# Kernel optimization log

Measured on AMD Instinct MI355X. Metric: run time of the kernel, lower is better.

Reference implementation:

```python
import jax, jax.numpy as jnp
import numpy as np

B, S, D, H = 2, 2048, 1024, 16
HD = D // H  # head dim = 64


def setup_inputs() -> dict:
    key = jax.random.key(0)
    ks = jax.random.split(key, 11)
    s = 0.02
    return {
        "query": jax.random.normal(ks[0], (B, S, D), jnp.float32),
        "key": jax.random.normal(ks[1], (B, S, D), jnp.float32),
        "value": jax.random.normal(ks[2], (B, S, D), jnp.float32),
        "Wq": jax.random.normal(ks[3], (D, D), jnp.float32) * s,
        "bq": jnp.zeros((D,), jnp.float32),
        "Wk": jax.random.normal(ks[4], (D, D), jnp.float32) * s,
        "bk": jnp.zeros((D,), jnp.float32),
        "Wv": jax.random.normal(ks[5], (D, D), jnp.float32) * s,
        "bv": jnp.zeros((D,), jnp.float32),
        "Wo": jax.random.normal(ks[6], (D, D), jnp.float32) * s,
        "bo": jnp.zeros((D,), jnp.float32),
    }


def reference(query, key, value, Wq, bq, Wk, bk, Wv, bv, Wo, bo):
    # Linear projections (torch Linear: x @ W^T + b; here W stored as [in, out])
    q = query @ Wq + bq  # [B,S,D]
    k = key @ Wk + bk
    v = value @ Wv + bv
    # split heads -> [B,H,S,HD]
    q = q.reshape(B, S, H, HD).transpose(0, 2, 1, 3)
    k = k.reshape(B, S, H, HD).transpose(0, 2, 1, 3)
    v = v.reshape(B, S, H, HD).transpose(0, 2, 1, 3)
    scores = jnp.einsum("bhqd,bhkd->bhqk", q, k) / jnp.sqrt(jnp.float32(HD))
    probs = jax.nn.softmax(scores, axis=-1)
    # dropout is identity at inference
    ctx = jnp.einsum("bhqk,bhkd->bhqd", probs, v)
    ctx = ctx.transpose(0, 2, 1, 3).reshape(B, S, D)
    return ctx @ Wo + bo
```

## Files before the change

kernel.cpp:

```cpp
#include <hip/hip_runtime.h>
#include <hip/hip_bf16.h>

#define BB 2
#define SS 2048
#define DD 1024
#define HH 16
#define HD 64
#define MM (BB*SS)

typedef __attribute__((ext_vector_type(8))) short bf16x8;
typedef __attribute__((ext_vector_type(4))) float f32x4;

static __device__ inline unsigned short f2bf(float x) {
    unsigned int u = __float_as_uint(x);
    unsigned int r = (u + 0x7fffu + ((u >> 16) & 1u)) >> 16;
    return (unsigned short)r;
}

static __device__ inline unsigned pack2bf(float lo, float hi) {
    union { __hip_bfloat162 h; unsigned u; } c;
    c.h = __float22bfloat162_rn(make_float2(lo, hi));
    return c.u;
}

static __device__ inline f32x4 mfma16(bf16x8 a, bf16x8 b, f32x4 c) {
    return __builtin_amdgcn_mfma_f32_16x16x32_bf16(a, b, c, 0, 0, 0);
}

static __device__ inline float fast_exp2(float x) {
    return __builtin_amdgcn_exp2f(x);
}

typedef __attribute__((address_space(3))) unsigned int lds_u32;
typedef const __attribute__((address_space(1))) unsigned int glb_u32;
static __device__ inline void async_ld16(const void* g, void* l) {
    __builtin_amdgcn_global_load_lds((glb_u32*)g, (lds_u32*)l, 16, 0, 0);
}

struct PrepArgs {
    const float* csrc[3];
    unsigned short* cdst[3];
    const float* wsrc[4];
    unsigned short* wdst[4];
};
__global__ __launch_bounds__(256) void prep_inputs(PrepArgs args) {
    const int z = blockIdx.z;
    const int t = threadIdx.x;
    if (z < 3) {
        const float* in = args.csrc[z];
        unsigned short* out = args.cdst[z];
        int chunk = (blockIdx.y * 32 + blockIdx.x) * 4096;
#pragma unroll
        for (int r = 0; r < 4; r++) {
            int i = chunk + r * 1024 + t * 4;
            float4 v = *(const float4*)(in + i);
            uint2 o;
            o.x = pack2bf(v.x, v.y);
            o.y = pack2bf(v.z, v.w);
            *(uint2*)(out + i) = o;
        }
    } else {
        __shared__ float tile[32][33];
        const float* in = args.wsrc[z - 3];
        unsigned short* out = args.wdst[z - 3];
        int c0 = blockIdx.x * 32, r0 = blockIdx.y * 32;
        int x = t & 31, y0 = t >> 5;
        for (int yy = y0; yy < 32; yy += 8)
            tile[yy][x] = in[(size_t)(r0 + yy) * DD + c0 + x];
        __syncthreads();
        for (int yy = y0; yy < 32; yy += 8)
            out[(size_t)(c0 + yy) * DD + r0 + x] = f2bf(tile[x][yy]);
    }
}

struct QKVArgs {
    const unsigned short* A[3];
    const unsigned short* Bt[3];
    const float* bias[3];
    unsigned short* C[3];
};

#define QSCALE 0.1803368801111204f

#define NBUF 4
#define NT (DD / 32)

__global__ __launch_bounds__(512, 2) void gemm_qkv(QKVArgs args) {
    __shared__ alignas(16) unsigned short AS[NBUF][256 * 32];
    __shared__ alignas(16) unsigned short BS[NBUF][256 * 32];
    const int z = blockIdx.z;
    const float scale = (z == 0) ? QSCALE : 1.0f;
    const unsigned short* __restrict__ A = args.A[z];
    const unsigned short* __restrict__ Bt = args.Bt[z];
    const float* __restrict__ bias = args.bias[z];
    unsigned short* __restrict__ C = args.C[z];
    const int K = DD, N = DD;
    const int t = threadIdx.x;
    const int lane = t & 63, wave = t >> 6;
    const int quad = lane >> 4, l15 = lane & 15;
    const int wm = wave & 1, wn = wave >> 1;
    const int m0 = blockIdx.y * 256, n0 = blockIdx.x * 256;

    const int srow = wave * 16 + (lane >> 2);
    const int sslot = (lane & 3) ^ ((lane >> 3) & 3);
    const unsigned short* gA0 = A + (size_t)(m0 + srow) * K + sslot * 8;
    const unsigned short* gA1 = gA0 + (size_t)128 * K;
    const unsigned short* gB0 = Bt + (size_t)(n0 + srow) * K + sslot * 8;
    const unsigned short* gB1 = gB0 + (size_t)128 * K;
    const int rlo = wave * 512;
    const int rhi = wave * 512 + 4096;

    const int swzq = quad ^ ((l15 >> 1) & 3);

    auto stage = [&](int kt) {
        const int b = kt & (NBUF - 1);
        const size_t ko = (size_t)kt * 32;
        async_ld16(gA0 + ko, &AS[b][rlo]);
        async_ld16(gA1 + ko, &AS[b][rhi]);
        async_ld16(gB0 + ko, &BS[b][rlo]);
        async_ld16(gB1 + ko, &BS[b][rhi]);
    };

    stage(0); stage(1); stage(2);

    f32x4 acc[8][4];
#pragma unroll
    for (int i = 0; i < 8; i++)
#pragma unroll
        for (int j = 0; j < 4; j++) acc[i][j] = (f32x4){0.f, 0.f, 0.f, 0.f};

#pragma unroll 4
    for (int kt = 0; kt < NT; ++kt) {
        if (kt < NT - 2)       asm volatile("s_waitcnt vmcnt(8)" ::: "memory");
        else if (kt == NT - 2) asm volatile("s_waitcnt vmcnt(4)" ::: "memory");
        else                   asm volatile("s_waitcnt vmcnt(0)" ::: "memory");
        __builtin_amdgcn_s_barrier();
        if (kt + 3 < NT) stage(kt + 3);

        const unsigned short* Ab = AS[kt & (NBUF - 1)];
        const unsigned short* Bb = BS[kt & (NBUF - 1)];
        bf16x8 af[8], bfr[4];
#pragma unroll
        for (int i = 0; i < 8; i++)
            af[i] = *(const bf16x8*)&Ab[(wm * 128 + i * 16 + l15) * 32 + swzq * 8];
#pragma unroll
        for (int j = 0; j < 4; j++)
            bfr[j] = *(const bf16x8*)&Bb[(wn * 64 + j * 16 + l15) * 32 + swzq * 8];

        __builtin_amdgcn_s_setprio(1);
#pragma unroll
        for (int i = 0; i < 8; i++)
#pragma unroll
            for (int j = 0; j < 4; j++)
                acc[i][j] = mfma16(af[i], bfr[j], acc[i][j]);
        __builtin_amdgcn_s_setprio(0);
    }

    if (z == 2) {
#pragma unroll
        for (int j = 0; j < 4; j++) {
            int col = n0 + wn * 64 + j * 16 + l15;
            float bv = bias[col];
#pragma unroll
            for (int i = 0; i < 8; i++) {
                int rowb = m0 + wm * 128 + i * 16 + quad * 4;
                int b = rowb >> 11, s = rowb & (SS - 1);
                uint2 w;
                w.x = pack2bf(acc[i][j][0] + bv, acc[i][j][1] + bv);
                w.y = pack2bf(acc[i][j][2] + bv, acc[i][j][3] + bv);
                *(uint2*)(C + (size_t)b * DD * SS + (size_t)col * SS + s) = w;
            }
        }
    } else {
#pragma unroll
        for (int j = 0; j < 4; j++) {
            int col = n0 + wn * 64 + j * 16 + l15;
            float bv = bias[col];
#pragma unroll
            for (int i = 0; i < 8; i++) {
                int rowb = m0 + wm * 128 + i * 16 + quad * 4;
#pragma unroll
                for (int rr = 0; rr < 4; rr++) {
                    float v = (acc[i][j][rr] + bv) * scale;
                    C[(size_t)(rowb + rr) * N + col] = f2bf(v);
                }
            }
        }
    }
}

__global__ __launch_bounds__(256) void gemm_out(const unsigned short* __restrict__ A,
                                                const unsigned short* __restrict__ Bt,
                                                const float* __restrict__ bias,
                                                float* __restrict__ C) {
    __shared__ alignas(16) unsigned short As[128 * 32];
    __shared__ alignas(16) unsigned short Bs[64 * 32];
    const int t = threadIdx.x;
    const int lane = t & 63, wave = t >> 6;
    const int quad = lane >> 4, l15 = lane & 15;
    const int m0 = blockIdx.y * 128, n0 = blockIdx.x * 64;
    const int K = DD, N = DD;

    const unsigned short* gA = A + (size_t)(m0 + wave * 16 + (lane >> 2)) * K + (lane & 3) * 8;
    const unsigned short* gB = Bt + (size_t)(n0 + wave * 16 + (lane >> 2)) * K + (lane & 3) * 8;
    unsigned short* lA0 = &As[(wave * 16) * 32];
    unsigned short* lA1 = &As[(wave * 16 + 64) * 32];
    unsigned short* lB0 = &Bs[(wave * 16) * 32];

    f32x4 acc[2][4];
#pragma unroll
    for (int i = 0; i < 2; i++)
#pragma unroll
        for (int j = 0; j < 4; j++) acc[i][j] = (f32x4){0.f, 0.f, 0.f, 0.f};

    for (int k0 = 0; k0 < K; k0 += 32) {
        __syncthreads();
        async_ld16(gA + k0, lA0);
        async_ld16(gA + (size_t)64 * K + k0, lA1);
        async_ld16(gB + k0, lB0);
        __syncthreads();

        bf16x8 af[2], bfr[4];
#pragma unroll
        for (int i = 0; i < 2; i++)
            af[i] = *(const bf16x8*)&As[(wave * 32 + i * 16 + l15) * 32 + quad * 8];
#pragma unroll
        for (int j = 0; j < 4; j++)
            bfr[j] = *(const bf16x8*)&Bs[(j * 16 + l15) * 32 + quad * 8];
#pragma unroll
        for (int i = 0; i < 2; i++)
#pragma unroll
            for (int j = 0; j < 4; j++)
                acc[i][j] = mfma16(af[i], bfr[j], acc[i][j]);
    }

#pragma unroll
    for (int j = 0; j < 4; j++) {
        int col = n0 + j * 16 + l15;
        float bv = bias[col];
#pragma unroll
        for (int i = 0; i < 2; i++) {
            int rowb = m0 + wave * 32 + i * 16 + quad * 4;
#pragma unroll
            for (int rr = 0; rr < 4; rr++)
                C[(size_t)(rowb + rr) * N + col] = acc[i][j][rr] + bv;
        }
    }
}

#define TK 64
#define NTILE (SS / TK)
#define LDP 72

__global__ __launch_bounds__(256, 2) void flash_attn(const unsigned short* __restrict__ Q,
                                                     const unsigned short* __restrict__ Kg,
                                                     const unsigned short* __restrict__ Vt,
                                                     unsigned short* __restrict__ ctx) {
    __shared__ alignas(16) unsigned short Ks[2][TK * LDP];
    __shared__ alignas(16) unsigned short Vs[2][TK * LDP];
    const int t = threadIdx.x;
    const int lane = t & 63, wave = t >> 6;
    const int quad = lane >> 4, l15 = lane & 15;
    const int qg = blockIdx.x & 15;
    const int bh = blockIdx.x >> 4;
    const int h = bh & 15, b = bh >> 4;
    const int q0 = (qg * 4 + wave) * 32;

    const unsigned short* Qb = Q + (size_t)b * SS * DD + h * HD;
    const unsigned short* Kb = Kg + (size_t)b * SS * DD + h * HD;
    const unsigned short* Vb = Vt + ((size_t)b * DD + h * HD) * SS;

    const int r0 = t >> 3, cs = t & 7;
    const unsigned short* gK = Kb + (size_t)r0 * DD + cs * 8;
    const unsigned short* gV = Vb + (size_t)r0 * SS + cs * 8;
    const int ldsoff0 = r0 * LDP + cs * 8;
    const int ldsoff1 = (r0 + 32) * LDP + cs * 8;

    bf16x8 qa[2][2];
#pragma unroll
    for (int qt = 0; qt < 2; qt++) {
        qa[qt][0] = *(const bf16x8*)(Qb + (size_t)(q0 + qt * 16 + l15) * DD + quad * 8);
        qa[qt][1] = *(const bf16x8*)(Qb + (size_t)(q0 + qt * 16 + l15) * DD + 32 + quad * 8);
    }

    float lrow[2] = {0.f, 0.f};
    f32x4 o[2][4];
#pragma unroll
    for (int qt = 0; qt < 2; qt++)
#pragma unroll
        for (int j = 0; j < 4; j++) o[qt][j] = (f32x4){0.f, 0.f, 0.f, 0.f};

    {
        uint4 kr0 = *(const uint4*)(gK);
        uint4 kr1 = *(const uint4*)(gK + (size_t)32 * DD);
        uint4 vr0 = *(const uint4*)(gV);
        uint4 vr1 = *(const uint4*)(gV + (size_t)32 * SS);
        *(uint4*)&Ks[0][ldsoff0] = kr0;
        *(uint4*)&Ks[0][ldsoff1] = kr1;
        *(uint4*)&Vs[0][ldsoff0] = vr0;
        *(uint4*)&Vs[0][ldsoff1] = vr1;
    }
    __syncthreads();

    for (int tile = 0; tile < NTILE; ++tile) {
        const int buf = tile & 1;
        uint4 kr0, kr1, vr0, vr1;
        if (tile + 1 < NTILE) {
            const unsigned short* gKn = gK + (size_t)(tile + 1) * TK * DD;
            const unsigned short* gVn = gV + (tile + 1) * TK;
            kr0 = *(const uint4*)(gKn);
            kr1 = *(const uint4*)(gKn + (size_t)32 * DD);
            vr0 = *(const uint4*)(gVn);
            vr1 = *(const uint4*)(gVn + (size_t)32 * SS);
        }
        const unsigned short* Ksb = Ks[buf];
        const unsigned short* Vsb = Vs[buf];
#pragma unroll
        for (int half = 0; half < 2; half++) {
            const int kb0 = half * 32;
            bf16x8 k0 = *(const bf16x8*)&Ksb[(kb0 + l15) * LDP + quad * 8];
            bf16x8 k1 = *(const bf16x8*)&Ksb[(kb0 + l15) * LDP + 32 + quad * 8];
            bf16x8 k2 = *(const bf16x8*)&Ksb[(kb0 + 16 + l15) * LDP + quad * 8];
            bf16x8 k3 = *(const bf16x8*)&Ksb[(kb0 + 16 + l15) * LDP + 32 + quad * 8];
            union { ushort4 s[2]; bf16x8 v; } af[4];
#pragma unroll
            for (int j = 0; j < 4; j++) {
                af[j].s[0] = *(const ushort4*)&Vsb[(j * 16 + l15) * LDP + kb0 + quad * 4];
                af[j].s[1] = *(const ushort4*)&Vsb[(j * 16 + l15) * LDP + kb0 + 16 + quad * 4];
            }
#pragma unroll
            for (int qt = 0; qt < 2; qt++) {
                f32x4 sc0 = (f32x4){0.f, 0.f, 0.f, 0.f};
                f32x4 sc1 = (f32x4){0.f, 0.f, 0.f, 0.f};
                sc0 = mfma16(k0, qa[qt][0], sc0);
                sc0 = mfma16(k1, qa[qt][1], sc0);
                sc1 = mfma16(k2, qa[qt][0], sc1);
                sc1 = mfma16(k3, qa[qt][1], sc1);

                float p[8];
#pragma unroll
                for (int rr = 0; rr < 4; rr++) {
                    p[rr]     = fast_exp2(sc0[rr]);
                    p[rr + 4] = fast_exp2(sc1[rr]);
                }
                lrow[qt] += (p[0] + p[1]) + (p[2] + p[3]) + (p[4] + p[5]) + (p[6] + p[7]);

                union { unsigned u[4]; bf16x8 v; } pf;
                pf.u[0] = pack2bf(p[0], p[1]);
                pf.u[1] = pack2bf(p[2], p[3]);
                pf.u[2] = pack2bf(p[4], p[5]);
                pf.u[3] = pack2bf(p[6], p[7]);

#pragma unroll
                for (int j = 0; j < 4; j++)
                    o[qt][j] = mfma16(af[j].v, pf.v, o[qt][j]);
            }
        }
        if (tile + 1 < NTILE) {
            __syncthreads();
            *(uint4*)&Ks[buf ^ 1][ldsoff0] = kr0;
            *(uint4*)&Ks[buf ^ 1][ldsoff1] = kr1;
            *(uint4*)&Vs[buf ^ 1][ldsoff0] = vr0;
            *(uint4*)&Vs[buf ^ 1][ldsoff1] = vr1;
            __syncthreads();
        }
    }

#pragma unroll
    for (int qt = 0; qt < 2; qt++) {
        float l = lrow[qt];
        l += __shfl_xor(l, 16, 64);
        l += __shfl_xor(l, 32, 64);
        float linv = 1.0f / l;
        unsigned short* crow = ctx + ((size_t)b * SS + q0 + qt * 16 + l15) * DD + h * HD;
#pragma unroll
        for (int j = 0; j < 4; j++) {
            uint2 w;
            w.x = pack2bf(o[qt][j][0] * linv, o[qt][j][1] * linv);
            w.y = pack2bf(o[qt][j][2] * linv, o[qt][j][3] * linv);
            *(uint2*)(crow + j * 16 + quad * 4) = w;
        }
    }
}

extern "C" void kernel_launch(void* const* d_in, const int* in_sizes, int n_in,
                              void* d_out, int out_size, void* d_ws, size_t ws_size,
                              hipStream_t stream) {
    const float* query = (const float*)d_in[0];
    const float* key   = (const float*)d_in[1];
    const float* value = (const float*)d_in[2];
    const float* Wq = (const float*)d_in[3];
    const float* bq = (const float*)d_in[4];
    const float* Wk = (const float*)d_in[5];
    const float* bk = (const float*)d_in[6];
    const float* Wv = (const float*)d_in[7];
    const float* bv = (const float*)d_in[8];
    const float* Wo = (const float*)d_in[9];
    const float* bo = (const float*)d_in[10];
    float* out = (float*)d_out;

    char* ws = (char*)d_ws;
    const size_t WSZ = (size_t)DD * DD * 2;
    const size_t XSZ = (size_t)MM * DD * 2;
    unsigned short* Wqt = (unsigned short*)(ws + 0 * WSZ);
    unsigned short* Wkt = (unsigned short*)(ws + 1 * WSZ);
    unsigned short* Wvt = (unsigned short*)(ws + 2 * WSZ);
    unsigned short* Wot = (unsigned short*)(ws + 3 * WSZ);
    unsigned short* Xq  = (unsigned short*)(ws + 4 * WSZ);
    unsigned short* Xk  = (unsigned short*)(ws + 4 * WSZ + 1 * XSZ);
    unsigned short* Xv  = (unsigned short*)(ws + 4 * WSZ + 2 * XSZ);
    unsigned short* Qp  = (unsigned short*)(ws + 4 * WSZ + 3 * XSZ);
    unsigned short* Kp  = (unsigned short*)(ws + 4 * WSZ + 4 * XSZ);
    unsigned short* Vtp = (unsigned short*)(ws + 4 * WSZ + 5 * XSZ);
    unsigned short* ctx = Xk;

    PrepArgs pargs;
    pargs.csrc[0] = query; pargs.csrc[1] = key; pargs.csrc[2] = value;
    pargs.cdst[0] = Xq; pargs.cdst[1] = Xk; pargs.cdst[2] = Xv;
    pargs.wsrc[0] = Wq; pargs.wsrc[1] = Wk; pargs.wsrc[2] = Wv; pargs.wsrc[3] = Wo;
    pargs.wdst[0] = Wqt; pargs.wdst[1] = Wkt; pargs.wdst[2] = Wvt; pargs.wdst[3] = Wot;
    prep_inputs<<<dim3(32, 32, 7), 256, 0, stream>>>(pargs);

    QKVArgs args;
    args.A[0] = Xq; args.A[1] = Xk; args.A[2] = Xv;
    args.Bt[0] = Wqt; args.Bt[1] = Wkt; args.Bt[2] = Wvt;
    args.bias[0] = bq; args.bias[1] = bk; args.bias[2] = bv;
    args.C[0] = Qp; args.C[1] = Kp; args.C[2] = Vtp;
    gemm_qkv<<<dim3(DD / 256, MM / 256, 3), 512, 0, stream>>>(args);

    flash_attn<<<BB * HH * 16, 256, 0, stream>>>(Qp, Kp, Vtp, ctx);

    gemm_out<<<dim3(DD / 64, MM / 128), 256, 0, stream>>>(ctx, Wot, bo, out);
}
```

Baseline: 230.8 us.

## Restructure QKV GEMM into 64-wide K tiles with interleaved load/MFMA phases

Replaces the 4-deep 32-wide K-tile ring buffer in the QKV projection GEMM with a double buffer of 64-wide K tiles. Each iteration is split into four quarter phases that read LDS fragments, issue async global loads for the next B or A halves, and run MFMA sub-blocks separated by barriers. This is an HK/8-wave ping-pong style schedule meant to overlap LDS reads, global prefetch and matrix math and to halve loop overhead. It adds many more barriers per iteration and uses a reworked XOR swizzle. The tighter buffer reuse risks races or stalls if the vmcnt accounting is off.

After: 227.6 us. Within noise of the previous version (-1.4%).

```diff
diff --git a/kernel.cpp b/kernel.cpp
--- a/kernel.cpp
+++ b/kernel.cpp
@@ -82,12 +82,11 @@
 
 #define QSCALE 0.1803368801111204f
 
-#define NBUF 4
-#define NT (DD / 32)
+#define NKT 16
 
 __global__ __launch_bounds__(512, 2) void gemm_qkv(QKVArgs args) {
-    __shared__ alignas(16) unsigned short AS[NBUF][256 * 32];
-    __shared__ alignas(16) unsigned short BS[NBUF][256 * 32];
+    __shared__ alignas(16) unsigned short AS[2][256 * 64];
+    __shared__ alignas(16) unsigned short BS[2][256 * 64];
     const int z = blockIdx.z;
     const float scale = (z == 0) ? QSCALE : 1.0f;
     const unsigned short* __restrict__ A = args.A[z];
@@ -101,27 +100,27 @@
     const int wm = wave & 1, wn = wave >> 1;
     const int m0 = blockIdx.y * 256, n0 = blockIdx.x * 256;
 
-    const int srow = wave * 16 + (lane >> 2);
-    const int sslot = (lane & 3) ^ ((lane >> 3) & 3);
-    const unsigned short* gA0 = A + (size_t)(m0 + srow) * K + sslot * 8;
-    const unsigned short* gA1 = gA0 + (size_t)128 * K;
-    const unsigned short* gB0 = Bt + (size_t)(n0 + srow) * K + sslot * 8;
-    const unsigned short* gB1 = gB0 + (size_t)128 * K;
-    const int rlo = wave * 512;
-    const int rhi = wave * 512 + 4096;
-
-    const int swzq = quad ^ ((l15 >> 1) & 3);
-
-    auto stage = [&](int kt) {
-        const int b = kt & (NBUF - 1);
-        const size_t ko = (size_t)kt * 32;
-        async_ld16(gA0 + ko, &AS[b][rlo]);
-        async_ld16(gA1 + ko, &AS[b][rhi]);
-        async_ld16(gB0 + ko, &BS[b][rlo]);
-        async_ld16(gB1 + ko, &BS[b][rhi]);
+    const int srow = t >> 3;
+    const int cslot = (t & 7) ^ (srow & 7);
+    const unsigned short* gA = A + (size_t)(m0 + srow) * K + cslot * 8;
+    const unsigned short* gB = Bt + (size_t)(n0 + srow) * K + cslot * 8;
+    const int dstoff = srow * 64 + (t & 7) * 8;
+
+    auto stageA = [&](int tl, int h) {
+        unsigned short* d = &AS[tl & 1][h * 128 * 64 + dstoff];
+        const unsigned short* s = gA + (size_t)(h * 128) * K + (size_t)tl * 64;
+        async_ld16(s, d);
+        async_ld16(s + (size_t)64 * K, d + 64 * 64);
     };
-
-    stage(0); stage(1); stage(2);
+    auto stageB = [&](int tl, int h) {
+        unsigned short* d = &BS[tl & 1][h * 128 * 64 + dstoff];
+        const unsigned short* s = gB + (size_t)(h * 128) * K + (size_t)tl * 64;
+        async_ld16(s, d);
+        async_ld16(s + (size_t)64 * K, d + 64 * 64);
+    };
+
+    stageA(0, 0); stageA(0, 1); stageB(0, 0); stageB(0, 1);
+    stageA(1, 0); stageA(1, 1);
 
     f32x4 acc[8][4];
 #pragma unroll
@@ -129,30 +128,93 @@
 #pragma unroll
         for (int j = 0; j < 4; j++) acc[i][j] = (f32x4){0.f, 0.f, 0.f, 0.f};
 
-#pragma unroll 4
-    for (int kt = 0; kt < NT; ++kt) {
-        if (kt < NT - 2)       asm volatile("s_waitcnt vmcnt(8)" ::: "memory");
-        else if (kt == NT - 2) asm volatile("s_waitcnt vmcnt(4)" ::: "memory");
-        else                   asm volatile("s_waitcnt vmcnt(0)" ::: "memory");
-        __builtin_amdgcn_s_barrier();
-        if (kt + 3 < NT) stage(kt + 3);
-
-        const unsigned short* Ab = AS[kt & (NBUF - 1)];
-        const unsigned short* Bb = BS[kt & (NBUF - 1)];
-        bf16x8 af[8], bfr[4];
-#pragma unroll
-        for (int i = 0; i < 8; i++)
-            af[i] = *(const bf16x8*)&Ab[(wm * 128 + i * 16 + l15) * 32 + swzq * 8];
-#pragma unroll
-        for (int j = 0; j < 4; j++)
-            bfr[j] = *(const bf16x8*)&Bb[(wn * 64 + j * 16 + l15) * 32 + swzq * 8];
-
+#pragma unroll 2
+    for (int kt = 0; kt < NKT; ++kt) {
+        if (kt < NKT - 1) asm volatile("s_waitcnt vmcnt(4)" ::: "memory");
+        else              asm volatile("s_waitcnt vmcnt(0)" ::: "memory");
+        __builtin_amdgcn_s_barrier();
+
+        const unsigned short* Ab = AS[kt & 1];
+        const unsigned short* Bb = BS[kt & 1];
+        bf16x8 af[4][2], bf[4][2];
+
+#pragma unroll
+        for (int i = 0; i < 4; i++) {
+            const int row = wm * 128 + i * 16 + l15;
+#pragma unroll
+            for (int kk = 0; kk < 2; kk++)
+                af[i][kk] = *(const bf16x8*)&Ab[row * 64 + ((kk * 4 + quad) ^ (l15 & 7)) * 8];
+        }
+#pragma unroll
+        for (int j = 0; j < 2; j++) {
+            const int row = wn * 64 + j * 16 + l15;
+#pragma unroll
+            for (int kk = 0; kk < 2; kk++)
+                bf[j][kk] = *(const bf16x8*)&Bb[row * 64 + ((kk * 4 + quad) ^ (l15 & 7)) * 8];
+        }
+        if (kt + 1 < NKT) stageB(kt + 1, 0);
+        __builtin_amdgcn_s_barrier();
         __builtin_amdgcn_s_setprio(1);
 #pragma unroll
-        for (int i = 0; i < 8; i++)
-#pragma unroll
-            for (int j = 0; j < 4; j++)
-                acc[i][j] = mfma16(af[i], bfr[j], acc[i][j]);
+        for (int i = 0; i < 4; i++)
+#pragma unroll
+            for (int j = 0; j < 2; j++) {
+                acc[i][j] = mfma16(af[i][0], bf[j][0], acc[i][j]);
+                acc[i][j] = mfma16(af[i][1], bf[j][1], acc[i][j]);
+            }
+        __builtin_amdgcn_s_setprio(0);
+        __builtin_amdgcn_s_barrier();
+
+#pragma unroll
+        for (int j = 2; j < 4; j++) {
+            const int row = wn * 64 + j * 16 + l15;
+#pragma unroll
+            for (int kk = 0; kk < 2; kk++)
+                bf[j][kk] = *(const bf16x8*)&Bb[row * 64 + ((kk * 4 + quad) ^ (l15 & 7)) * 8];
+        }
+        if (kt + 1 < NKT) stageB(kt + 1, 1);
+        __builtin_amdgcn_s_barrier();
+        __builtin_amdgcn_s_setprio(1);
+#pragma unroll
+        for (int i = 0; i < 4; i++)
+#pragma unroll
+            for (int j = 2; j < 4; j++) {
+                acc[i][j] = mfma16(af[i][0], bf[j][0], acc[i][j]);
+                acc[i][j] = mfma16(af[i][1], bf[j][1], acc[i][j]);
+            }
+        __builtin_amdgcn_s_setprio(0);
+        __builtin_amdgcn_s_barrier();
+
+#pragma unroll
+        for (int i = 0; i < 4; i++) {
+            const int row = wm * 128 + 64 + i * 16 + l15;
+#pragma unroll
+            for (int kk = 0; kk < 2; kk++)
+                af[i][kk] = *(const bf16x8*)&Ab[row * 64 + ((kk * 4 + quad) ^ (l15 & 7)) * 8];
+        }
+        if (kt + 2 < NKT) stageA(kt + 2, 0);
+        __builtin_amdgcn_s_barrier();
+        __builtin_amdgcn_s_setprio(1);
+#pragma unroll
+        for (int i = 0; i < 4; i++)
+#pragma unroll
+            for (int j = 0; j < 2; j++) {
+                acc[4 + i][j] = mfma16(af[i][0], bf[j][0], acc[4 + i][j]);
+                acc[4 + i][j] = mfma16(af[i][1], bf[j][1], acc[4 + i][j]);
+            }
+        __builtin_amdgcn_s_setprio(0);
+        __builtin_amdgcn_s_barrier();
+
+        if (kt + 2 < NKT) stageA(kt + 2, 1);
+        __builtin_amdgcn_s_barrier();
+        __builtin_amdgcn_s_setprio(1);
+#pragma unroll
+        for (int i = 0; i < 4; i++)
+#pragma unroll
+            for (int j = 2; j < 4; j++) {
+                acc[4 + i][j] = mfma16(af[i][0], bf[j][0], acc[4 + i][j]);
+                acc[4 + i][j] = mfma16(af[i][1], bf[j][1], acc[4 + i][j]);
+            }
         __builtin_amdgcn_s_setprio(0);
     }
 
```
